# Kernel optimization log

Hardware: AMD Instinct MI355X
Metric: run time of the kernel (lower is better)

The kernel has to match this reference:

```python
import jax, jax.numpy as jnp
import numpy as np

B, D, C = 1024, 512, 100000
S, M = 64.0, 0.1
EPS = 1e-12  # torch F.normalize eps


def setup_inputs() -> dict:
    key = jax.random.key(0)
    k1, k2, k3 = jax.random.split(key, 3)
    inputs = jax.random.normal(k1, (B, D), dtype=jnp.float32)
    labels = jax.random.randint(k2, (B,), 0, C, dtype=jnp.int64)
    weight = jax.random.normal(k3, (C, D), dtype=jnp.float32)
    return {"inputs": inputs, "labels": labels, "weight": weight}


def _l2norm(x):
    # matches F.normalize: x / max(||x||, eps)
    n = jnp.sqrt(jnp.sum(x * x, axis=-1, keepdims=True))
    return x / jnp.maximum(n, EPS)


def reference(inputs, labels, weight):
    # cosine similarity: [B, C]
    cos_theta = jnp.clip(_l2norm(inputs) @ _l2norm(weight).T, -1.0, 1.0)
    theta = jnp.arccos(cos_theta)
    # add margin m only at the label column (one-hot scatter without materializing one_hot)
    rows = jnp.arange(theta.shape[0])
    theta_m = theta.at[rows, labels].add(M)
    logits = S * jnp.cos(theta_m)
    # cross-entropy (mean reduction)
    logp = jax.nn.log_softmax(logits, axis=-1)
    loss = -jnp.mean(logp[rows, labels])
    return loss
```

## Files before the change

### kernel.cpp

```cpp
#include <hip/hip_runtime.h>
#include <hip/hip_bf16.h>
#include <stdint.h>

#define DIM 512
#define NROWS 1024
#define NCLS 100000
#define NCLS_PAD 100032
#define SCALE_S 64.0f
#define NBN 192
#define NSTRIPE ((NCLS + 63) / 64)

typedef __attribute__((ext_vector_type(8))) __bf16 bf16x8;
typedef __attribute__((ext_vector_type(4))) float f32x4;

__device__ __forceinline__ unsigned short f2bf(float x) {
  __hip_bfloat16 h = __float2bfloat16(x);
  union { __hip_bfloat16 h; unsigned short u; } v; v.h = h; return v.u;
}
__device__ __forceinline__ unsigned pack2(float a, float b) {
  return ((unsigned)f2bf(b) << 16) | (unsigned)f2bf(a);
}
__device__ __forceinline__ void async_ld16(const void* g, void* l) {
  __builtin_amdgcn_global_load_lds((const __attribute__((address_space(1))) void*)g,
                                   (__attribute__((address_space(3))) void*)l, 16, 0, 0);
}

__global__ void prep_a(const float* __restrict__ X, unsigned short* __restrict__ A16,
                       float* __restrict__ xnorm) {
  const int row = blockIdx.x;
  const int lane = threadIdx.x;
  const float4* xp = (const float4*)(X + (size_t)row * DIM);
  float4 v0 = xp[lane];
  float4 v1 = xp[lane + 64];
  float ss = v0.x*v0.x + v0.y*v0.y + v0.z*v0.z + v0.w*v0.w
           + v1.x*v1.x + v1.y*v1.y + v1.z*v1.z + v1.w*v1.w;
  #pragma unroll
  for (int m = 1; m < 64; m <<= 1) ss += __shfl_xor(ss, m);
  const float nrm = sqrtf(ss);
  const float inv = 1.0f / fmaxf(nrm, 1e-12f);
  if (lane == 0) xnorm[row] = nrm;
  unsigned short* ap = A16 + (size_t)row * DIM;
  *(uint2*)(ap + lane * 4)       = make_uint2(pack2(v0.x*inv, v0.y*inv), pack2(v0.z*inv, v0.w*inv));
  *(uint2*)(ap + 256 + lane * 4) = make_uint2(pack2(v1.x*inv, v1.y*inv), pack2(v1.z*inv, v1.w*inv));
}

__global__ void prep_w(const float* __restrict__ Wg, unsigned short* __restrict__ W16) {
  const int row = blockIdx.x * 4 + (threadIdx.x >> 6);
  const int lane = threadIdx.x & 63;
  unsigned short* op = W16 + (size_t)row * DIM;
  if (row >= NCLS) {
    *(uint4*)((char*)op + lane * 16) = make_uint4(0, 0, 0, 0);
    return;
  }
  const float4* xp = (const float4*)(Wg + (size_t)row * DIM);
  float4 v0 = xp[lane];
  float4 v1 = xp[lane + 64];
  float ss = v0.x*v0.x + v0.y*v0.y + v0.z*v0.z + v0.w*v0.w
           + v1.x*v1.x + v1.y*v1.y + v1.z*v1.z + v1.w*v1.w;
  #pragma unroll
  for (int m = 1; m < 64; m <<= 1) ss += __shfl_xor(ss, m);
  const float inv = 1.0f / fmaxf(sqrtf(ss), 1e-12f);
  *(uint2*)(op + lane * 4)       = make_uint2(pack2(v0.x*inv, v0.y*inv), pack2(v0.z*inv, v0.w*inv));
  *(uint2*)(op + 256 + lane * 4) = make_uint2(pack2(v1.x*inv, v1.y*inv), pack2(v1.z*inv, v1.w*inv));
}


__device__ __forceinline__ void stage_w(const char* W16g, char* wldsb, int buf, int ktp,
                                        int tcol0, int wave, int lane) {
  #pragma unroll
  for (int it = 0; it < 2; ++it) {
    const int d = (wave * 2 + it) * 1024 + lane * 16;
    const int c = d >> 7;
    const int b = d & 127;
    async_ld16(W16g + ((size_t)(tcol0 + c) * 1024 + ktp * 128 + (b ^ ((c & 7) << 4))),
               wldsb + buf * 8192 + (wave * 2 + it) * 1024);
  }
}

template<int KT>
__device__ __forceinline__ void mfma_phase(const char* wldsb, const bf16x8 (&af)[8][2][2],
                                           f32x4 (&acc)[2][4], int lr, int lg) {
  const char* wb = wldsb + KT * 8192;
  #pragma unroll
  for (int kh = 0; kh < 2; ++kh) {
    bf16x8 bfr[4];
    #pragma unroll
    for (int ni = 0; ni < 4; ++ni) {
      const int bc = ni * 16 + lr;
      const int o = (bc * 128 + kh * 64 + lg * 16) ^ ((bc & 7) << 4);
      bfr[ni] = *(const bf16x8*)(wb + o);
    }
    #pragma unroll
    for (int mi = 0; mi < 2; ++mi)
      #pragma unroll
      for (int ni = 0; ni < 4; ++ni)
        acc[mi][ni] = __builtin_amdgcn_mfma_f32_16x16x32_bf16(af[KT][kh][mi], bfr[ni], acc[mi][ni], 0, 0, 0);
  }
}

#define PHASE(KT, VMT)                                                              \
  do {                                                                              \
    if ((KT) < 2) {                                                                 \
      stage_w(W16g, wldsb, ((KT) + 6) & 7, (KT) + 6, col0, wave, lane);             \
      asm volatile("s_waitcnt vmcnt(12)" ::: "memory");                             \
    } else if (has_next) {                                                          \
      stage_w(W16g, wldsb, ((KT) + 6) & 7, (KT) - 2, ncol0, wave, lane);            \
      asm volatile("s_waitcnt vmcnt(12)" ::: "memory");                             \
    } else {                                                                        \
      asm volatile("s_waitcnt vmcnt(" #VMT ")" ::: "memory");                       \
    }                                                                               \
    __builtin_amdgcn_s_barrier();                                                   \
    mfma_phase<(KT)>(wldsb, af, acc, lr, lg);                                       \
  } while (0)

__global__ __launch_bounds__(256, 2) void gemm_lse2(
    const unsigned short* __restrict__ A16, const unsigned short* __restrict__ W16,
    float* __restrict__ part_s) {
  __shared__ char wlds[8 * 8192];
  char* wldsb = wlds;
  const char* W16g = (const char*)W16;

  const int tid = threadIdx.x;
  const int lane = tid & 63;
  const int wave = tid >> 6;
  const int lr = lane & 15, lg = lane >> 4;
  const int bid = blockIdx.x;
  const int mblk = (bid >> 3) & 7;
  const int nblk = ((bid >> 6) << 3) + (bid & 7);

  bf16x8 af[8][2][2];
  {
    const char* Ab = (const char*)A16 + (size_t)(mblk * 128 + wave * 32) * 1024;
    #pragma unroll
    for (int kt = 0; kt < 8; ++kt)
      #pragma unroll
      for (int kh = 0; kh < 2; ++kh)
        #pragma unroll
        for (int mi = 0; mi < 2; ++mi)
          af[kt][kh][mi] = *(const bf16x8*)(Ab + (size_t)(mi * 16 + lr) * 1024 + kt * 128 + kh * 64 + lg * 16);
  }

  f32x4 acc[2][4];
  #pragma unroll
  for (int mi = 0; mi < 2; ++mi)
    #pragma unroll
    for (int ni = 0; ni < 4; ++ni) acc[mi][ni] = f32x4{0.f, 0.f, 0.f, 0.f};
  float srow[2][4];
  #pragma unroll
  for (int mi = 0; mi < 2; ++mi)
    #pragma unroll
    for (int r = 0; r < 4; ++r) srow[mi][r] = 0.f;

  {
    const int c0 = nblk * 64;
    #pragma unroll
    for (int pk = 0; pk < 6; ++pk) stage_w(W16g, wldsb, pk, pk, c0, wave, lane);
  }

  for (int s = nblk; s < NSTRIPE; s += NBN) {
    const int col0 = s * 64;
    const int ncol0 = (s + NBN) * 64;
    const bool has_next = (s + NBN) < NSTRIPE;

    PHASE(0, 12); PHASE(1, 12); PHASE(2, 10); PHASE(3, 8);
    PHASE(4, 6);  PHASE(5, 4);  PHASE(6, 2);  PHASE(7, 0);

    #pragma unroll
    for (int mi = 0; mi < 2; ++mi)
      #pragma unroll
      for (int ni = 0; ni < 4; ++ni) {
        const bool ok = (col0 + ni * 16 + lr) < NCLS;
        #pragma unroll
        for (int r = 0; r < 4; ++r) {
          float v = acc[mi][ni][r] * SCALE_S;
          v = fminf(SCALE_S, fmaxf(-SCALE_S, v));
          srow[mi][r] += ok ? __expf(v - SCALE_S) : 0.f;
          acc[mi][ni][r] = 0.f;
        }
      }
  }

  #pragma unroll
  for (int mi = 0; mi < 2; ++mi)
    #pragma unroll
    for (int r = 0; r < 4; ++r) {
      float v = srow[mi][r];
      v += __shfl_xor(v, 1); v += __shfl_xor(v, 2);
      v += __shfl_xor(v, 4); v += __shfl_xor(v, 8);
      if (lr == 0)
        part_s[(size_t)nblk * NROWS + mblk * 128 + wave * 32 + mi * 16 + lg * 4 + r] = v;
    }
}

__global__ void finalize_kernel(const float* __restrict__ X, const int* __restrict__ labels,
                                const float* __restrict__ Wg, const float* __restrict__ xnorm,
                                const float* __restrict__ part_s, float* __restrict__ rowloss) {
  const int row = blockIdx.x;
  const int lane = threadIdx.x;
  const int lbl = labels[row];
  const float4* xp = (const float4*)(X + (size_t)row * DIM);
  const float4* wp = (const float4*)(Wg + (size_t)lbl * DIM);
  float dot = 0.f, wss = 0.f;
  #pragma unroll
  for (int i = 0; i < 2; ++i) {
    float4 xv = xp[lane + 64 * i];
    float4 wv = wp[lane + 64 * i];
    dot += xv.x*wv.x + xv.y*wv.y + xv.z*wv.z + xv.w*wv.w;
    wss += wv.x*wv.x + wv.y*wv.y + wv.z*wv.z + wv.w*wv.w;
  }
  float psum = 0.f;
  #pragma unroll
  for (int i = 0; i < NBN / 64; ++i)
    psum += part_s[(size_t)(lane + 64 * i) * NROWS + row];
  #pragma unroll
  for (int m = 1; m < 64; m <<= 1) {
    dot += __shfl_xor(dot, m); wss += __shfl_xor(wss, m); psum += __shfl_xor(psum, m);
  }
  if (lane == 0) {
    float c = dot / (fmaxf(xnorm[row], 1e-12f) * fmaxf(sqrtf(wss), 1e-12f));
    c = fminf(1.f, fmaxf(-1.f, c));
    const float cm = 0.99500416527802576610f;
    const float sn = 0.09983341664682815230f;
    float unmod = SCALE_S * c;
    float modv  = SCALE_S * (c * cm - sqrtf(fmaxf(0.f, 1.f - c * c)) * sn);
    float stot = psum - __expf(unmod - SCALE_S) + __expf(modv - SCALE_S);
    stot = fmaxf(stot, 1e-37f);
    rowloss[row] = (logf(stot) + SCALE_S) - modv;
  }
}

__global__ void reduce_kernel(const float* __restrict__ rowloss, float* __restrict__ out) {
  const int tid = threadIdx.x;
  float s = 0.f;
  #pragma unroll
  for (int i = 0; i < 4; ++i) s += rowloss[tid + i * 256];
  #pragma unroll
  for (int m = 1; m < 64; m <<= 1) s += __shfl_xor(s, m);
  __shared__ float wsum[4];
  if ((tid & 63) == 0) wsum[tid >> 6] = s;
  __syncthreads();
  if (tid == 0) out[0] = (wsum[0] + wsum[1] + wsum[2] + wsum[3]) * (1.0f / NROWS);
}

extern "C" void kernel_launch(void* const* d_in, const int* in_sizes, int n_in,
                              void* d_out, int out_size, void* d_ws, size_t ws_size,
                              hipStream_t stream) {
  const float* X      = (const float*)d_in[0];
  const int*   labels = (const int*)d_in[1];
  const float* Wg     = (const float*)d_in[2];
  float* out = (float*)d_out;
  char* ws = (char*)d_ws;
  unsigned short* A16 = (unsigned short*)ws;
  unsigned short* W16 = (unsigned short*)(ws + 1048576);
  float* part_s  = (float*)(ws + 103481344);
  float* xnorm   = (float*)(ws + 104267776);
  float* rowloss = (float*)(ws + 104271872);

  prep_a<<<NROWS, 64, 0, stream>>>(X, A16, xnorm);
  prep_w<<<NCLS_PAD / 4, 256, 0, stream>>>(Wg, W16);
  gemm_lse2<<<NBN * 8, 256, 0, stream>>>(A16, W16, part_s);
  finalize_kernel<<<NROWS, 64, 0, stream>>>(X, labels, Wg, xnorm, part_s, rowloss);
  reduce_kernel<<<1, 256, 0, stream>>>(rowloss, out);
}
```

Before: 164.5 us.

## Rewrite logit GEMM with 256x256 tiles staging A and W through double-buffered LDS

Replaces the 128x64-tile GEMM, which held the A rows in registers, with a 512-thread block computing a 256x256 output tile. Both A and W k-slices are streamed into a double-buffered LDS ring. A persistent grid of 256 blocks walks 391 column stripes, and per-block row sums are reduced across waves in LDS, so finalize now sums only 64 partials. The exp is rewritten as exp2 of a fused multiply-add. The column-validity mask is dropped and the padded zero columns are left in the sum, adding tiny exp(-64) terms. The bigger tile is meant to cut global/LDS traffic per MFMA, at the cost of 128KB of LDS (one block per CU) and uneven stripe counts across blocks.

```diff
diff --git a/kernel.cpp b/kernel.cpp
--- a/kernel.cpp
+++ b/kernel.cpp
@@ -5,10 +5,11 @@
 #define DIM 512
 #define NROWS 1024
 #define NCLS 100000
-#define NCLS_PAD 100032
+#define NST 391
+#define NCLS_PAD (NST * 256)
 #define SCALE_S 64.0f
-#define NBN 192
-#define NSTRIPE ((NCLS + 63) / 64)
+#define NBN 64
+#define S_LOG2E 92.332482616893662f
 
 typedef __attribute__((ext_vector_type(8))) __bf16 bf16x8;
 typedef __attribute__((ext_vector_type(4))) float f32x4;
@@ -65,131 +66,134 @@
 }
 
 
-__device__ __forceinline__ void stage_w(const char* W16g, char* wldsb, int buf, int ktp,
-                                        int tcol0, int wave, int lane) {
-  #pragma unroll
-  for (int it = 0; it < 2; ++it) {
-    const int d = (wave * 2 + it) * 1024 + lane * 16;
-    const int c = d >> 7;
+__device__ __forceinline__ void stage_tile(const char* Ab, const char* W16g,
+                                           long col0, int kt, int slot,
+                                           int wave, int lane, char* lds) {
+  char* dstA = lds + slot * 65536;
+  char* dstB = dstA + 32768;
+  const char* Wb = W16g + (size_t)col0 * 1024;
+  #pragma unroll
+  for (int it = 0; it < 4; ++it) {
+    const int chunk = wave * 4 + it;
+    const int d = chunk * 1024 + lane * 16;
+    const int row = d >> 7;
     const int b = d & 127;
-    async_ld16(W16g + ((size_t)(tcol0 + c) * 1024 + ktp * 128 + (b ^ ((c & 7) << 4))),
-               wldsb + buf * 8192 + (wave * 2 + it) * 1024);
-  }
-}
-
-template<int KT>
-__device__ __forceinline__ void mfma_phase(const char* wldsb, const bf16x8 (&af)[8][2][2],
-                                           f32x4 (&acc)[2][4], int lr, int lg) {
-  const char* wb = wldsb + KT * 8192;
+    const int srel = row * 1024 + kt * 128 + (b ^ ((row & 7) << 4));
+    async_ld16(Ab + srel, dstA + chunk * 1024);
+    async_ld16(Wb + srel, dstB + chunk * 1024);
+  }
+}
+
+__device__ __forceinline__ void compute_tile(const char* lds, int slot, int wr, int wn,
+                                             int lr, int lg, f32x4 (&acc)[8][4]) {
+  const char* Ab = lds + slot * 65536;
+  const char* Bb = Ab + 32768;
   #pragma unroll
   for (int kh = 0; kh < 2; ++kh) {
-    bf16x8 bfr[4];
+    bf16x8 afr[8]; bf16x8 bfr[4];
+    #pragma unroll
+    for (int mi = 0; mi < 8; ++mi) {
+      const int row = wr * 128 + mi * 16 + lr;
+      afr[mi] = *(const bf16x8*)(Ab + row * 128 + ((kh * 64 + lg * 16) ^ ((row & 7) << 4)));
+    }
     #pragma unroll
     for (int ni = 0; ni < 4; ++ni) {
-      const int bc = ni * 16 + lr;
-      const int o = (bc * 128 + kh * 64 + lg * 16) ^ ((bc & 7) << 4);
-      bfr[ni] = *(const bf16x8*)(wb + o);
-    }
-    #pragma unroll
-    for (int mi = 0; mi < 2; ++mi)
+      const int col = wn * 64 + ni * 16 + lr;
+      bfr[ni] = *(const bf16x8*)(Bb + col * 128 + ((kh * 64 + lg * 16) ^ ((col & 7) << 4)));
+    }
+    #pragma unroll
+    for (int mi = 0; mi < 8; ++mi)
       #pragma unroll
       for (int ni = 0; ni < 4; ++ni)
-        acc[mi][ni] = __builtin_amdgcn_mfma_f32_16x16x32_bf16(af[KT][kh][mi], bfr[ni], acc[mi][ni], 0, 0, 0);
-  }
-}
-
-#define PHASE(KT, VMT)                                                              \
-  do {                                                                              \
-    if ((KT) < 2) {                                                                 \
-      stage_w(W16g, wldsb, ((KT) + 6) & 7, (KT) + 6, col0, wave, lane);             \
-      asm volatile("s_waitcnt vmcnt(12)" ::: "memory");                             \
-    } else if (has_next) {                                                          \
-      stage_w(W16g, wldsb, ((KT) + 6) & 7, (KT) - 2, ncol0, wave, lane);            \
-      asm volatile("s_waitcnt vmcnt(12)" ::: "memory");                             \
-    } else {                                                                        \
-      asm volatile("s_waitcnt vmcnt(" #VMT ")" ::: "memory");                       \
-    }                                                                               \
-    __builtin_amdgcn_s_barrier();                                                   \
-    mfma_phase<(KT)>(wldsb, af, acc, lr, lg);                                       \
-  } while (0)
-
-__global__ __launch_bounds__(256, 2) void gemm_lse2(
+        acc[mi][ni] = __builtin_amdgcn_mfma_f32_16x16x32_bf16(afr[mi], bfr[ni], acc[mi][ni], 0, 0, 0);
+  }
+}
+
+__global__ __launch_bounds__(512, 2) void gemm_lse3(
     const unsigned short* __restrict__ A16, const unsigned short* __restrict__ W16,
     float* __restrict__ part_s) {
-  __shared__ char wlds[8 * 8192];
-  char* wldsb = wlds;
+  __shared__ char lds[2 * 65536];
   const char* W16g = (const char*)W16;
 
   const int tid = threadIdx.x;
   const int lane = tid & 63;
   const int wave = tid >> 6;
   const int lr = lane & 15, lg = lane >> 4;
+  const int wr = wave >> 2;
+  const int wn = wave & 3;
+
   const int bid = blockIdx.x;
-  const int mblk = (bid >> 3) & 7;
-  const int nblk = ((bid >> 6) << 3) + (bid & 7);
-
-  bf16x8 af[8][2][2];
-  {
-    const char* Ab = (const char*)A16 + (size_t)(mblk * 128 + wave * 32) * 1024;
-    #pragma unroll
-    for (int kt = 0; kt < 8; ++kt)
+  const int x = bid & 7;
+  const int q = bid >> 3;
+  const int mblk = q & 3;
+  const int nblk = x * 8 + (q >> 2);
+  const int mrow0 = mblk * 256;
+
+  const char* Ab = (const char*)A16 + (size_t)mrow0 * 1024;
+
+  f32x4 acc[8][4];
+  #pragma unroll
+  for (int mi = 0; mi < 8; ++mi)
+    #pragma unroll
+    for (int ni = 0; ni < 4; ++ni) acc[mi][ni] = f32x4{0.f, 0.f, 0.f, 0.f};
+  float srow[8][4];
+  #pragma unroll
+  for (int mi = 0; mi < 8; ++mi)
+    #pragma unroll
+    for (int r = 0; r < 4; ++r) srow[mi][r] = 0.f;
+
+  long s = nblk;
+  long col0 = s * 256;
+  stage_tile(Ab, W16g, col0, 0, 0, wave, lane, lds);
+
+  while (true) {
+    const bool more = (s + NBN) < NST;
+    const long ncol0 = (s + NBN) * 256;
+
+    #pragma unroll
+    for (int t = 0; t < 8; ++t) {
+      __builtin_amdgcn_s_barrier();
+      if (t < 7)      stage_tile(Ab, W16g, col0, t + 1, (t + 1) & 1, wave, lane, lds);
+      else if (more)  stage_tile(Ab, W16g, ncol0, 0, 0, wave, lane, lds);
+      if (t == 7 && !more) { asm volatile("s_waitcnt vmcnt(0)" ::: "memory"); }
+      else                 { asm volatile("s_waitcnt vmcnt(8)" ::: "memory"); }
+      __builtin_amdgcn_s_barrier();
+      compute_tile(lds, t & 1, wr, wn, lr, lg, acc);
+    }
+
+    #pragma unroll
+    for (int mi = 0; mi < 8; ++mi)
       #pragma unroll
-      for (int kh = 0; kh < 2; ++kh)
-        #pragma unroll
-        for (int mi = 0; mi < 2; ++mi)
-          af[kt][kh][mi] = *(const bf16x8*)(Ab + (size_t)(mi * 16 + lr) * 1024 + kt * 128 + kh * 64 + lg * 16);
-  }
-
-  f32x4 acc[2][4];
-  #pragma unroll
-  for (int mi = 0; mi < 2; ++mi)
-    #pragma unroll
-    for (int ni = 0; ni < 4; ++ni) acc[mi][ni] = f32x4{0.f, 0.f, 0.f, 0.f};
-  float srow[2][4];
-  #pragma unroll
-  for (int mi = 0; mi < 2; ++mi)
-    #pragma unroll
-    for (int r = 0; r < 4; ++r) srow[mi][r] = 0.f;
-
-  {
-    const int c0 = nblk * 64;
-    #pragma unroll
-    for (int pk = 0; pk < 6; ++pk) stage_w(W16g, wldsb, pk, pk, c0, wave, lane);
-  }
-
-  for (int s = nblk; s < NSTRIPE; s += NBN) {
-    const int col0 = s * 64;
-    const int ncol0 = (s + NBN) * 64;
-    const bool has_next = (s + NBN) < NSTRIPE;
-
-    PHASE(0, 12); PHASE(1, 12); PHASE(2, 10); PHASE(3, 8);
-    PHASE(4, 6);  PHASE(5, 4);  PHASE(6, 2);  PHASE(7, 0);
-
-    #pragma unroll
-    for (int mi = 0; mi < 2; ++mi)
-      #pragma unroll
-      for (int ni = 0; ni < 4; ++ni) {
-        const bool ok = (col0 + ni * 16 + lr) < NCLS;
+      for (int ni = 0; ni < 4; ++ni)
         #pragma unroll
         for (int r = 0; r < 4; ++r) {
-          float v = acc[mi][ni][r] * SCALE_S;
-          v = fminf(SCALE_S, fmaxf(-SCALE_S, v));
-          srow[mi][r] += ok ? __expf(v - SCALE_S) : 0.f;
+          float c = fminf(1.f, fmaxf(-1.f, acc[mi][ni][r]));
+          srow[mi][r] += exp2f(fmaf(c, S_LOG2E, -S_LOG2E));
           acc[mi][ni][r] = 0.f;
         }
-      }
-  }
-
-  #pragma unroll
-  for (int mi = 0; mi < 2; ++mi)
+
+    if (!more) break;
+    s += NBN; col0 = ncol0;
+  }
+
+  float* ldsrow = (float*)lds;
+  __builtin_amdgcn_s_barrier();
+  #pragma unroll
+  for (int mi = 0; mi < 8; ++mi)
     #pragma unroll
     for (int r = 0; r < 4; ++r) {
       float v = srow[mi][r];
       v += __shfl_xor(v, 1); v += __shfl_xor(v, 2);
       v += __shfl_xor(v, 4); v += __shfl_xor(v, 8);
       if (lr == 0)
-        part_s[(size_t)nblk * NROWS + mblk * 128 + wave * 32 + mi * 16 + lg * 4 + r] = v;
-    }
+        ldsrow[wn * 256 + wr * 128 + mi * 16 + lg * 4 + r] = v;
+    }
+  __builtin_amdgcn_s_barrier();
+  asm volatile("s_waitcnt lgkmcnt(0)" ::: "memory");
+  if (tid < 256) {
+    float v = ldsrow[tid] + ldsrow[256 + tid] + ldsrow[512 + tid] + ldsrow[768 + tid];
+    part_s[(size_t)nblk * NROWS + mrow0 + tid] = v;
+  }
 }
 
 __global__ void finalize_kernel(const float* __restrict__ X, const int* __restrict__ labels,
@@ -208,10 +212,7 @@
     dot += xv.x*wv.x + xv.y*wv.y + xv.z*wv.z + xv.w*wv.w;
     wss += wv.x*wv.x + wv.y*wv.y + wv.z*wv.z + wv.w*wv.w;
   }
-  float psum = 0.f;
-  #pragma unroll
-  for (int i = 0; i < NBN / 64; ++i)
-    psum += part_s[(size_t)(lane + 64 * i) * NROWS + row];
+  float psum = part_s[(size_t)lane * NROWS + row];
   #pragma unroll
   for (int m = 1; m < 64; m <<= 1) {
     dot += __shfl_xor(dot, m); wss += __shfl_xor(wss, m); psum += __shfl_xor(psum, m);
@@ -252,13 +253,13 @@
   char* ws = (char*)d_ws;
   unsigned short* A16 = (unsigned short*)ws;
   unsigned short* W16 = (unsigned short*)(ws + 1048576);
-  float* part_s  = (float*)(ws + 103481344);
-  float* xnorm   = (float*)(ws + 104267776);
-  float* rowloss = (float*)(ws + 104271872);
+  float* part_s  = (float*)(ws + 103546880);
+  float* xnorm   = (float*)(ws + 103809024);
+  float* rowloss = (float*)(ws + 103813120);
 
   prep_a<<<NROWS, 64, 0, stream>>>(X, A16, xnorm);
   prep_w<<<NCLS_PAD / 4, 256, 0, stream>>>(Wg, W16);
-  gemm_lse2<<<NBN * 8, 256, 0, stream>>>(A16, W16, part_s);
+  gemm_lse3<<<256, 512, 0, stream>>>(A16, W16, part_s);
   finalize_kernel<<<NROWS, 64, 0, stream>>>(X, labels, Wg, xnorm, part_s, rowloss);
   reduce_kernel<<<1, 256, 0, stream>>>(rowloss, out);
 }
```

Result: slower. 303.2 us (+84.3%).
